# Kernel optimization log

Measured on AMD Instinct MI355X. Metric: run time of the kernel, lower is better.

The kernel has to match this reference:

```python
import jax, jax.numpy as jnp
import numpy as np

B, H, W, C = 16, 64, 64, 256
HEADS, WS, SHIFTS, QD = 8, 8, (0, 4), 512
N = WS * WS
HD = C // HEADS
MLP_H = 4 * C
DEPTH = 2
EPS = 1e-5


def _rel_pos_index():
    coords = np.stack(np.meshgrid(np.arange(WS), np.arange(WS), indexing='ij'))  # [2,ws,ws]
    flat = coords.reshape(2, -1)
    rel = (flat[:, :, None] - flat[:, None, :]).transpose(1, 2, 0)  # [N,N,2]
    rel[..., 0] += WS - 1
    rel[..., 1] += WS - 1
    rel[..., 0] *= 2 * WS - 1
    return jnp.asarray(rel.sum(-1))  # [N,N] int


def _shift_mask(shift):
    img = np.zeros((H, W))
    cnt = 0
    for hs in (slice(0, -WS), slice(-WS, -shift), slice(-shift, None)):
        for ws_ in (slice(0, -WS), slice(-WS, -shift), slice(-shift, None)):
            img[hs, ws_] = cnt
            cnt += 1
    mw = img.reshape(H // WS, WS, W // WS, WS).transpose(0, 2, 1, 3).reshape(-1, N)  # [nW,N]
    am = mw[:, None, :] - mw[:, :, None]
    return jnp.asarray(np.where(am != 0, -100.0, 0.0).astype(np.float32))  # [nW,N,N]


RPI = _rel_pos_index()


def layernorm(x, g, b):
    mu = x.mean(-1, keepdims=True)
    var = ((x - mu) ** 2).mean(-1, keepdims=True)
    return (x - mu) * jax.lax.rsqrt(var + EPS) * g + b


def window_partition(x):  # [B,H,W,C] -> [B*nW, N, C]
    x = x.reshape(B, H // WS, WS, W // WS, WS, C)
    return x.transpose(0, 1, 3, 2, 4, 5).reshape(-1, N, C)


def window_reverse(w):  # [B*nW, N, C] -> [B,H,W,C]
    x = w.reshape(B, H // WS, W // WS, WS, WS, C)
    return x.transpose(0, 1, 3, 2, 4, 5).reshape(B, H, W, C)


def swin_block(x, shift, n1g, n1b, qkvw, qkvb, rpb, pw, pb, n2g, n2b, f1w, f1b, f2w, f2b):
    shortcut = x
    y = layernorm(x, n1g, n1b).reshape(B, H, W, C)
    if shift > 0:
        y = jnp.roll(y, (-shift, -shift), axis=(1, 2))
    xw = window_partition(y)                                      # [B_, N, C]
    qkv = (xw @ qkvw + qkvb).reshape(-1, N, 3, HEADS, HD)
    q, k, v = (qkv[:, :, i].transpose(0, 2, 1, 3) for i in range(3))  # [B_,h,N,hd]
    scores = jnp.einsum('bhnd,bhmd->bhnm', q * (HD ** -0.5), k)
    bias = rpb[RPI].transpose(2, 0, 1)                            # [h,N,N]
    scores = scores + bias[None]
    if shift > 0:
        mask = _shift_mask(shift)                                 # [nW,N,N]
        nW = mask.shape[0]
        scores = scores.reshape(B, nW, HEADS, N, N) + mask[None, :, None]
        scores = scores.reshape(-1, HEADS, N, N)
    attn = jax.nn.softmax(scores, axis=-1)
    out = jnp.einsum('bhnm,bhmd->bhnd', attn, v).transpose(0, 2, 1, 3).reshape(-1, N, C)
    out = out @ pw + pb
    y = window_reverse(out)
    if shift > 0:
        y = jnp.roll(y, (shift, shift), axis=(1, 2))
    x = shortcut + y.reshape(B, H * W, C)
    h = layernorm(x, n2g, n2b)
    h = jax.nn.gelu(h @ f1w + f1b, approximate=False) @ f2w + f2b
    return x + h


def cross_attn(x, cond, cng, cnb, inw, inb, outw, outb):
    xn = layernorm(x, cng, cnb)
    q = xn @ inw[:C].T + inb[:C]
    k = cond @ inw[C:2 * C].T + inb[C:2 * C]
    v = cond @ inw[2 * C:].T + inb[2 * C:]
    Tq, Tk = q.shape[1], k.shape[1]
    q = q.reshape(B, Tq, HEADS, HD).transpose(0, 2, 1, 3) * (HD ** -0.5)
    k = k.reshape(B, Tk, HEADS, HD).transpose(0, 2, 1, 3)
    v = v.reshape(B, Tk, HEADS, HD).transpose(0, 2, 1, 3)
    a = jax.nn.softmax(jnp.einsum('bhqd,bhkd->bhqk', q, k), axis=-1)
    o = jnp.einsum('bhqk,bhkd->bhqd', a, v).transpose(0, 2, 1, 3).reshape(B, Tq, C)
    return x + o @ outw.T + outb


def setup_inputs() -> dict:
    key = jax.random.key(0)
    ks = iter(jax.random.split(key, 40))
    s = 0.02
    d = {
        'x': jax.random.normal(next(ks), (B, H * W, C), jnp.float32),
        'emb': jax.random.normal(next(ks), (B, 1, QD), jnp.float32),
        'qenc_w': jax.random.normal(next(ks), (QD, C)) * s,
        'qenc_b': jnp.zeros((C,)),
        'n1_g': jnp.ones((DEPTH, C)), 'n1_b': jnp.zeros((DEPTH, C)),
        'qkv_w': jax.random.normal(next(ks), (DEPTH, C, 3 * C)) * s,
        'qkv_b': jnp.zeros((DEPTH, 3 * C)),
        'rpb': jax.random.normal(next(ks), (DEPTH, (2 * WS - 1) ** 2, HEADS)) * s,
        'proj_w': jax.random.normal(next(ks), (DEPTH, C, C)) * s,
        'proj_b': jnp.zeros((DEPTH, C)),
        'n2_g': jnp.ones((DEPTH, C)), 'n2_b': jnp.zeros((DEPTH, C)),
        'fc1_w': jax.random.normal(next(ks), (DEPTH, C, MLP_H)) * s,
        'fc1_b': jnp.zeros((DEPTH, MLP_H)),
        'fc2_w': jax.random.normal(next(ks), (DEPTH, MLP_H, C)) * s,
        'fc2_b': jnp.zeros((DEPTH, C)),
        'cn_g': jnp.ones((DEPTH, C)), 'cn_b': jnp.zeros((DEPTH, C)),
        'ca_in_w': jax.random.normal(next(ks), (DEPTH, 3 * C, C)) * s,
        'ca_in_b': jnp.zeros((DEPTH, 3 * C)),
        'ca_out_w': jax.random.normal(next(ks), (DEPTH, C, C)) * s,
        'ca_out_b': jnp.zeros((DEPTH, C)),
    }
    return d


def reference(x, emb, qenc_w, qenc_b, n1_g, n1_b, qkv_w, qkv_b, rpb, proj_w, proj_b,
              n2_g, n2_b, fc1_w, fc1_b, fc2_w, fc2_b, cn_g, cn_b,
              ca_in_w, ca_in_b, ca_out_w, ca_out_b):
    for d in range(DEPTH):
        x = swin_block(x, SHIFTS[d], n1_g[d], n1_b[d], qkv_w[d], qkv_b[d], rpb[d],
                       proj_w[d], proj_b[d], n2_g[d], n2_b[d],
                       fc1_w[d], fc1_b[d], fc2_w[d], fc2_b[d])
        cond = emb @ qenc_w + qenc_b  # recomputed per block as in original
        x = cross_attn(x, cond, cn_g[d], cn_b[d], ca_in_w[d], ca_in_b[d],
                       ca_out_w[d], ca_out_b[d])
    return x
```

## Files before the change

### kernel.cpp

```cpp
#include <hip/hip_runtime.h>


typedef unsigned short bfraw;
typedef short s16x8 __attribute__((ext_vector_type(8)));
typedef short s16x4 __attribute__((ext_vector_type(4)));
typedef float f32x4 __attribute__((ext_vector_type(4)));

#define DEV static __device__ __forceinline__

DEV float b2f(int u){
  union { unsigned int i; float f; } x;
  x.i = ((unsigned int)u & 0xffffu) << 16;
  return x.f;
}
DEV unsigned short f2bbits(float f){
  union { float f; unsigned int i; } x; x.f = f;
  unsigned int i = x.i;
  unsigned int lsb = (i >> 16) & 1u;
  i += 0x7fffu + lsb;
  return (unsigned short)(i >> 16);
}
DEV unsigned int pkbf(float lo, float hi){
  unsigned int r;
  asm("v_cvt_pk_bf16_f32 %0, %1, %2" : "=v"(r) : "v"(lo), "v"(hi));
  return r;
}
DEV float gelu_tanh(float x){
  float t2 = 1.5957691216057308f * fmaf(0.044715f * x * x, x, x);
  float e = __expf(-t2);
  return x * __builtin_amdgcn_rcpf(1.f + e);
}

#define GLOAD_LDS16(g, l) __builtin_amdgcn_global_load_lds(                      \
    (const __attribute__((address_space(1))) void*)(g),                          \
    (__attribute__((address_space(3))) void*)(l), 16, 0, 0)

__global__ void k_tr(const float* __restrict__ in, bfraw* __restrict__ out, int K, int N){
  int idx = blockIdx.x * 256 + threadIdx.x;
  if (idx >= K * N) return;
  int n = idx / K, k = idx - n * K;
  out[idx] = f2bbits(in[(size_t)k * N + n]);
}

__global__ __launch_bounds__(256) void k_ln(
    const float* __restrict__ x, const float* __restrict__ g,
    const float* __restrict__ b, bfraw* __restrict__ y)
{
  const int lane = threadIdx.x & 63, wv = threadIdx.x >> 6;
  const size_t row = (size_t)blockIdx.x * 4 + wv;
  const float4 v = *(const float4*)(x + row * 256 + lane * 4);
  float s  = v.x + v.y + v.z + v.w;
  float s2 = v.x*v.x + v.y*v.y + v.z*v.z + v.w*v.w;
#pragma unroll
  for (int off = 32; off; off >>= 1){
    s  += __shfl_xor(s,  off);
    s2 += __shfl_xor(s2, off);
  }
  float mu  = s * (1.f/256.f);
  float var = s2 * (1.f/256.f) - mu * mu;
  float rs  = rsqrtf(var + 1e-5f);
  const float4 gv = *(const float4*)(g + lane * 4);
  const float4 bv = *(const float4*)(b + lane * 4);
  uint2 o;
  o.x = pkbf((v.x - mu) * rs * gv.x + bv.x, (v.y - mu) * rs * gv.y + bv.y);
  o.y = pkbf((v.z - mu) * rs * gv.z + bv.z, (v.w - mu) * rs * gv.w + bv.w);
  *(uint2*)(y + row * 256 + lane * 4) = o;
}

template<int EPI>
__global__ __launch_bounds__(256, 2) void k_gemm(
    const bfraw* __restrict__ A, const bfraw* __restrict__ Bt,
    const float* __restrict__ bias,
    bfraw* __restrict__ Cout, int ldc,
    float* __restrict__ xfp, const float* __restrict__ xin,
    const float* __restrict__ addv,
    int M, int N, int K, int shift)
{
  constexpr int BK = 64;
  __shared__ __align__(16) bfraw sA[128 * BK];
  __shared__ __align__(16) bfraw sB[128 * BK];
  const int tid = threadIdx.x, lane = tid & 63, w = tid >> 6;
  const int lo16 = lane & 15, hg = lane >> 4;
  const int nbm = M >> 7, nbn = N >> 7;
  const int nwg = nbm * nbn;
  const int bid = blockIdx.x;
  const int wgid = (bid & 7) * (nwg >> 3) + (bid >> 3);
  const int tn = wgid % nbn, tm = wgid / nbn;
  const int m0 = tm << 7, n0 = tn << 7;
  const int wm = w & 1, wn = w >> 1;
  f32x4 acc[4][4] = {};

  const int srow = (w << 5) + (lane >> 3);
  const int scol = (((lane & 7) ^ (lane >> 3)) << 3);
  const int ksw  = (lane & 7) << 3;
  const bfraw* gA = A  + (size_t)(m0 + srow) * K + scol;
  const bfraw* gB = Bt + (size_t)(n0 + srow) * K + scol;

  const int cb = n0 + (wn << 6) + 4 * hg;

  f32x4 bv4[4];
#pragma unroll
  for (int ni = 0; ni < 4; ++ni) bv4[ni] = *(const f32x4*)(bias + cb + ni * 16);
  size_t rowoff_[4];
  f32x4 pre[16], pav[4];
  if constexpr (EPI == 2 || EPI == 3){
#pragma unroll
    for (int mi = 0; mi < 4; ++mi){
      const int r = m0 + (wm << 6) + (mi << 4) + lo16;
      if constexpr (EPI == 2){
        int b_ = r >> 12, rem = r & 4095;
        int wi = rem >> 6, n_ = rem & 63;
        int gi = ((wi >> 3) * 8 + (n_ >> 3) + shift) & 63;
        int gj = ((wi & 7) * 8 + (n_ & 7) + shift) & 63;
        rowoff_[mi] = ((size_t)b_ << 12) + gi * 64 + gj;
      } else {
        rowoff_[mi] = (size_t)r;
      }
      const float* src = (EPI == 2 ? xin : (const float*)xfp) + rowoff_[mi] * 256 + cb;
#pragma unroll
      for (int ni = 0; ni < 4; ++ni)
        pre[mi * 4 + ni] = *(const f32x4*)(src + ni * 16);
    }
    if constexpr (EPI == 3){
      const float* av = addv + (size_t)(m0 >> 12) * 256 + cb;
#pragma unroll
      for (int ni = 0; ni < 4; ++ni) pav[ni] = *(const f32x4*)(av + ni * 16);
    }
  }

  for (int kt = 0; kt < K; kt += BK){
    __syncthreads();
#pragma unroll
    for (int i = 0; i < 4; ++i){
      GLOAD_LDS16(gA + (size_t)(i * 8) * K + kt, &sA[(w * 4 + i) * 512]);
      GLOAD_LDS16(gB + (size_t)(i * 8) * K + kt, &sB[(w * 4 + i) * 512]);
    }
    __syncthreads();
#pragma unroll
    for (int ks = 0; ks < 2; ++ks){
      const int ko = (ks * 32 + (hg << 3)) ^ ksw;
      s16x8 af[4], bfr[4];
#pragma unroll
      for (int i = 0; i < 4; ++i){
        af[i]  = *(const s16x8*)&sA[((wm << 6) + (i << 4) + lo16) * BK + ko];
        bfr[i] = *(const s16x8*)&sB[((wn << 6) + (i << 4) + lo16) * BK + ko];
      }
#pragma unroll
      for (int ni = 0; ni < 4; ++ni)
#pragma unroll
        for (int mi = 0; mi < 4; ++mi)
          acc[ni][mi] = __builtin_amdgcn_mfma_f32_16x16x32_bf16(
              bfr[ni], af[mi], acc[ni][mi], 0, 0, 0);
    }
  }

#pragma unroll
  for (int mi = 0; mi < 4; ++mi){
    if constexpr (EPI == 0 || EPI == 1){
      const int r = m0 + (wm << 6) + (mi << 4) + lo16;
      bfraw* crow = Cout + (size_t)r * ldc + cb;
#pragma unroll
      for (int ni = 0; ni < 4; ++ni){
        f32x4 v = acc[ni][mi] + bv4[ni];
        if constexpr (EPI == 1){
          v[0] = gelu_tanh(v[0]); v[1] = gelu_tanh(v[1]);
          v[2] = gelu_tanh(v[2]); v[3] = gelu_tanh(v[3]);
        }
        uint2 o = make_uint2(pkbf(v[0], v[1]), pkbf(v[2], v[3]));
        *(uint2*)(crow + ni * 16) = o;
      }
    } else if constexpr (EPI == 2){
      float* xo = xfp + rowoff_[mi] * 256 + cb;
#pragma unroll
      for (int ni = 0; ni < 4; ++ni)
        *(f32x4*)(xo + ni * 16) = acc[ni][mi] + bv4[ni] + pre[mi * 4 + ni];
    } else {
      float* xo = xfp + rowoff_[mi] * 256 + cb;
#pragma unroll
      for (int ni = 0; ni < 4; ++ni)
        *(f32x4*)(xo + ni * 16) = acc[ni][mi] + bv4[ni] + pre[mi * 4 + ni] + pav[ni];
    }
  }
}

__global__ __launch_bounds__(64) void k_bias(const float* __restrict__ rpb,
                                             float* __restrict__ biasPk)
{
  const int blk = blockIdx.x;
  const int d = blk >> 5, cls = (blk >> 3) & 3, h = blk & 7;
  const int l = threadIdx.x, lo16 = l & 15, hg = l >> 4;
  const float* rp = rpb + (size_t)d * 225 * 8;
  float* ob = biasPk + (((size_t)d * 4 + cls) * 8 + h) * 4096;
#pragma unroll
  for (int mi = 0; mi < 4; ++mi)
#pragma unroll
    for (int ni = 0; ni < 4; ++ni)
#pragma unroll
      for (int j = 0; j < 4; ++j){
        int k = 16 * mi + 4 * hg + j, q = 16 * ni + lo16;
        int qr = q >> 3, qc = q & 7, kr = k >> 3, kc = k & 7;
        float v = rp[((qr - kr + 7) * 15 + (qc - kc + 7)) * 8 + h];
        if (d == 1){
          int lq = ((cls >> 1) ? (qr < 4 ? 1 : 2) : 0) * 3 + ((cls & 1) ? (qc < 4 ? 1 : 2) : 0);
          int lk = ((cls >> 1) ? (kr < 4 ? 1 : 2) : 0) * 3 + ((cls & 1) ? (kc < 4 ? 1 : 2) : 0);
          if (lq != lk) v -= 100.f;
        }
        ob[(mi * 4 + ni) * 256 + l * 4 + j] = v;
      }
}

__global__ __launch_bounds__(64) void k_attn(
    const bfraw* __restrict__ qkv, const float* __restrict__ biasPk,
    bfraw* __restrict__ aout, int shift)
{
  __shared__ __align__(16) bfraw sV[64 * 32];
  __shared__ __align__(16) bfraw sP[64 * 64];
  const int win = blockIdx.x >> 3, h = blockIdx.x & 7;
  const int b = win >> 6, wr = (win >> 3) & 7, wc = win & 7;
  const int l = threadIdx.x, lo16 = l & 15, hg = l >> 4;

  auto grow_of = [&](int n) -> size_t {
    int gi = (wr * 8 + (n >> 3) + shift) & 63;
    int gj = (wc * 8 + (n & 7) + shift) & 63;
    return ((size_t)b << 12) + gi * 64 + gj;
  };

  s16x8 vreg[4];
#pragma unroll
  for (int i = 0; i < 4; ++i){
    int row = i * 16 + (l >> 2);
    vreg[i] = *(const s16x8*)(qkv + grow_of(row) * 768 + 512 + h * 32 + (l & 3) * 8);
  }
#pragma unroll
  for (int i = 0; i < 4; ++i)
    *(s16x8*)&sV[i * 512 + l * 8] = vreg[i];

  s16x8 aK[4], bQ[4];
#pragma unroll
  for (int t = 0; t < 4; ++t){
    const bfraw* base = qkv + grow_of(16 * t + lo16) * 768 + h * 32 + hg * 8;
    bQ[t] = *(const s16x8*)base;
    aK[t] = *(const s16x8*)(base + 256);
  }

  f32x4 acc[4][4] = {};
#pragma unroll
  for (int mi = 0; mi < 4; ++mi)
#pragma unroll
    for (int ni = 0; ni < 4; ++ni)
      acc[mi][ni] = __builtin_amdgcn_mfma_f32_16x16x32_bf16(aK[mi], bQ[ni], acc[mi][ni], 0, 0, 0);

  const int cls = ((wr == 7) ? 2 : 0) | ((wc == 7) ? 1 : 0);
  const float* bb = biasPk + ((size_t)(cls * 8 + h)) * 4096;
#pragma unroll
  for (int mi = 0; mi < 4; ++mi)
#pragma unroll
    for (int ni = 0; ni < 4; ++ni){
      f32x4 bv4 = *(const f32x4*)(bb + (mi * 4 + ni) * 256 + l * 4);
      acc[mi][ni] = acc[mi][ni] * 0.17677669529663689f + bv4;
    }

#pragma unroll
  for (int ni = 0; ni < 4; ++ni){
    float m = acc[0][ni][0];
#pragma unroll
    for (int mi = 0; mi < 4; ++mi)
#pragma unroll
      for (int j = 0; j < 4; ++j) m = fmaxf(m, acc[mi][ni][j]);
    m = fmaxf(m, __shfl_xor(m, 16));
    m = fmaxf(m, __shfl_xor(m, 32));
    float s = 0.f;
#pragma unroll
    for (int mi = 0; mi < 4; ++mi)
#pragma unroll
      for (int j = 0; j < 4; ++j){
        float e = __expf(acc[mi][ni][j] - m);
        acc[mi][ni][j] = e; s += e;
      }
    s += __shfl_xor(s, 16);
    s += __shfl_xor(s, 32);
    float inv = 1.f / s;
#pragma unroll
    for (int mi = 0; mi < 4; ++mi)
#pragma unroll
      for (int j = 0; j < 4; ++j) acc[mi][ni][j] *= inv;
  }

#pragma unroll
  for (int mi = 0; mi < 4; ++mi)
#pragma unroll
    for (int ni = 0; ni < 4; ++ni){
      unsigned int w0 = pkbf(acc[mi][ni][0], acc[mi][ni][1]);
      unsigned int w1 = pkbf(acc[mi][ni][2], acc[mi][ni][3]);
      int q = 16 * ni + lo16;
      int ad = (q * 128 + (16 * mi + 4 * hg) * 2) ^ ((q & 7) << 4);
      *(uint2*)((char*)sP + ad) = make_uint2(w0, w1);
    }

  asm volatile("s_waitcnt lgkmcnt(0)" ::: "memory");
  __builtin_amdgcn_sched_barrier(0);

  f32x4 opv[4][2] = {};
#pragma unroll
  for (int kt = 0; kt < 2; ++kt){
    s16x8 ap[4];
#pragma unroll
    for (int qi = 0; qi < 4; ++qi){
      int q = 16 * qi + lo16;
      int ad = (q * 128 + (kt * 32 + hg * 8) * 2) ^ ((q & 7) << 4);
      ap[qi] = *(const s16x8*)((const char*)sP + ad);
    }
    s16x8 vb[2];
#pragma unroll
    for (int nt = 0; nt < 2; ++nt)
#pragma unroll
      for (int e = 0; e < 8; ++e)
        vb[nt][e] = (short)sV[(kt * 32 + hg * 8 + e) * 32 + nt * 16 + lo16];
#pragma unroll
    for (int qi = 0; qi < 4; ++qi)
#pragma unroll
      for (int nt = 0; nt < 2; ++nt)
        opv[qi][nt] = __builtin_amdgcn_mfma_f32_16x16x32_bf16(ap[qi], vb[nt], opv[qi][nt], 0, 0, 0);
  }

  bfraw* ob = aout + ((size_t)win * 64) * 256 + h * 32 + lo16;
#pragma unroll
  for (int qi = 0; qi < 4; ++qi)
#pragma unroll
    for (int nt = 0; nt < 2; ++nt)
#pragma unroll
      for (int j = 0; j < 4; ++j)
        ob[(size_t)(16 * qi + 4 * hg + j) * 256 + nt * 16] = f2bbits(opv[qi][nt][j]);
}

__global__ __launch_bounds__(256) void k_addvec(
    const float* __restrict__ emb, const float* __restrict__ qw, const float* __restrict__ qb,
    const float* __restrict__ inw, const float* __restrict__ inb,
    const float* __restrict__ outw, const float* __restrict__ outb,
    float* __restrict__ addv)
{
  const int d = blockIdx.x >> 4, b = blockIdx.x & 15;
  const int j = threadIdx.x;
  __shared__ float sc[256], sv[256];
  float a = qb[j];
  for (int k = 0; k < 512; ++k) a = fmaf(emb[b * 512 + k], qw[k * 256 + j], a);
  sc[j] = a; __syncthreads();
  float v = inb[d * 768 + 512 + j];
  const float* wrp = inw + (size_t)d * 768 * 256 + (size_t)(512 + j) * 256;
  for (int k = 0; k < 256; ++k) v = fmaf(sc[k], wrp[k], v);
  sv[j] = v; __syncthreads();
  float o = outb[d * 256 + j];
  const float* wop = outw + (size_t)d * 65536 + (size_t)j * 256;
  for (int k = 0; k < 256; ++k) o = fmaf(sv[k], wop[k], o);
  addv[(size_t)(d * 16 + b) * 256 + j] = o;
}

extern "C" void kernel_launch(void* const* d_in, const int* in_sizes, int n_in,
                              void* d_out, int out_size, void* d_ws, size_t ws_size,
                              hipStream_t stream)
{
  (void)in_sizes; (void)n_in; (void)out_size; (void)ws_size;
  const float* x_in     = (const float*)d_in[0];
  const float* emb      = (const float*)d_in[1];
  const float* qenc_w   = (const float*)d_in[2];
  const float* qenc_b   = (const float*)d_in[3];
  const float* n1_g     = (const float*)d_in[4];
  const float* n1_b     = (const float*)d_in[5];
  const float* qkv_w    = (const float*)d_in[6];
  const float* qkv_b    = (const float*)d_in[7];
  const float* rpb      = (const float*)d_in[8];
  const float* proj_w   = (const float*)d_in[9];
  const float* proj_b   = (const float*)d_in[10];
  const float* n2_g     = (const float*)d_in[11];
  const float* n2_b     = (const float*)d_in[12];
  const float* fc1_w    = (const float*)d_in[13];
  const float* fc1_b    = (const float*)d_in[14];
  const float* fc2_w    = (const float*)d_in[15];
  const float* fc2_b    = (const float*)d_in[16];
  const float* ca_in_w  = (const float*)d_in[19];
  const float* ca_in_b  = (const float*)d_in[20];
  const float* ca_out_w = (const float*)d_in[21];
  const float* ca_out_b = (const float*)d_in[22];

  float* xfp  = (float*)d_out;
  char* ws = (char*)d_ws;
  bfraw* ybuf = (bfraw*)ws;
  bfraw* qkvb = (bfraw*)(ws + ((size_t)32 << 20));
  bfraw* wT   = (bfraw*)(ws + ((size_t)160 << 20));
  float* biasPk = (float*)(ws + ((size_t)166 << 20));

  bfraw *qkvT[2], *projT[2], *fc1T[2], *fc2T[2];
  size_t off = 0;
  for (int d = 0; d < 2; ++d){ qkvT[d] = wT + off; off += 768 * 256; }
  for (int d = 0; d < 2; ++d){ projT[d] = wT + off; off += 256 * 256; }
  for (int d = 0; d < 2; ++d){ fc1T[d] = wT + off; off += 1024 * 256; }
  for (int d = 0; d < 2; ++d){ fc2T[d] = wT + off; off += 256 * 1024; }
  float* addv = (float*)(wT + ((off + 1) & ~(size_t)1));

  for (int d = 0; d < 2; ++d){
    k_tr<<<(256 * 768  + 255) / 256, 256, 0, stream>>>(qkv_w  + (size_t)d * 256 * 768,  qkvT[d], 256, 768);
    k_tr<<<(256 * 256  + 255) / 256, 256, 0, stream>>>(proj_w + (size_t)d * 256 * 256,  projT[d], 256, 256);
    k_tr<<<(256 * 1024 + 255) / 256, 256, 0, stream>>>(fc1_w  + (size_t)d * 256 * 1024, fc1T[d], 256, 1024);
    k_tr<<<(1024 * 256 + 255) / 256, 256, 0, stream>>>(fc2_w  + (size_t)d * 1024 * 256, fc2T[d], 1024, 256);
  }
  k_bias<<<64, 64, 0, stream>>>(rpb, biasPk);
  k_addvec<<<32, 256, 0, stream>>>(emb, qenc_w, qenc_b, ca_in_w, ca_in_b, ca_out_w, ca_out_b, addv);

  for (int d = 0; d < 2; ++d){
    const int shift = d ? 4 : 0;
    const float* resid_in = d ? (const float*)xfp : x_in;
    k_ln<<<16384, 256, 0, stream>>>(resid_in, n1_g + d * 256, n1_b + d * 256, ybuf);
    k_gemm<0><<<512 * 6, 256, 0, stream>>>(ybuf, qkvT[d], qkv_b + d * 768, qkvb, 768,
                                           nullptr, nullptr, nullptr, 65536, 768, 256, 0);
    k_attn<<<8192, 64, 0, stream>>>(qkvb, biasPk + (size_t)d * 4 * 8 * 4096, ybuf, shift);
    k_gemm<2><<<512 * 2, 256, 0, stream>>>(ybuf, projT[d], proj_b + d * 256, nullptr, 0,
                                           xfp, resid_in, nullptr, 65536, 256, 256, shift);
    k_ln<<<16384, 256, 0, stream>>>(xfp, n2_g + d * 256, n2_b + d * 256, ybuf);
    k_gemm<1><<<512 * 8, 256, 0, stream>>>(ybuf, fc1T[d], fc1_b + d * 1024, qkvb, 1024,
                                           nullptr, nullptr, nullptr, 65536, 1024, 256, 0);
    k_gemm<3><<<512 * 2, 256, 0, stream>>>(qkvb, fc2T[d], fc2_b + d * 256, nullptr, 0,
                                           xfp, nullptr, addv + (size_t)d * 16 * 256,
                                           65536, 256, 1024, 0);
  }
}
```

Measured before the change: 687.9 us.

## Fuse MLP fc1+GELU+fc2 into one kernel keeping hidden activations in LDS

Replaces the two MLP GEMM launches with a single k_mlp kernel. Each block processes 64 rows, computes the fc1 hidden chunk with GELU into LDS, and accumulates fc2 directly, then adds bias, the cross-attention vector and the residual. This removes the global write and read of the large 4C hidden tensor. In exchange, weights are loaded from global memory per warp without LDS staging, and there are fewer, larger blocks.

```diff
diff --git a/kernel.cpp b/kernel.cpp
--- a/kernel.cpp
+++ b/kernel.cpp
@@ -73,7 +73,6 @@
     const float* __restrict__ bias,
     bfraw* __restrict__ Cout, int ldc,
     float* __restrict__ xfp, const float* __restrict__ xin,
-    const float* __restrict__ addv,
     int M, int N, int K, int shift)
 {
   constexpr int BK = 64;
@@ -102,29 +101,20 @@
 #pragma unroll
   for (int ni = 0; ni < 4; ++ni) bv4[ni] = *(const f32x4*)(bias + cb + ni * 16);
   size_t rowoff_[4];
-  f32x4 pre[16], pav[4];
-  if constexpr (EPI == 2 || EPI == 3){
+  f32x4 pre[16];
+  if constexpr (EPI == 2){
 #pragma unroll
     for (int mi = 0; mi < 4; ++mi){
       const int r = m0 + (wm << 6) + (mi << 4) + lo16;
-      if constexpr (EPI == 2){
-        int b_ = r >> 12, rem = r & 4095;
-        int wi = rem >> 6, n_ = rem & 63;
-        int gi = ((wi >> 3) * 8 + (n_ >> 3) + shift) & 63;
-        int gj = ((wi & 7) * 8 + (n_ & 7) + shift) & 63;
-        rowoff_[mi] = ((size_t)b_ << 12) + gi * 64 + gj;
-      } else {
-        rowoff_[mi] = (size_t)r;
-      }
-      const float* src = (EPI == 2 ? xin : (const float*)xfp) + rowoff_[mi] * 256 + cb;
+      int b_ = r >> 12, rem = r & 4095;
+      int wi = rem >> 6, n_ = rem & 63;
+      int gi = ((wi >> 3) * 8 + (n_ >> 3) + shift) & 63;
+      int gj = ((wi & 7) * 8 + (n_ & 7) + shift) & 63;
+      rowoff_[mi] = ((size_t)b_ << 12) + gi * 64 + gj;
+      const float* src = xin + rowoff_[mi] * 256 + cb;
 #pragma unroll
       for (int ni = 0; ni < 4; ++ni)
         pre[mi * 4 + ni] = *(const f32x4*)(src + ni * 16);
-    }
-    if constexpr (EPI == 3){
-      const float* av = addv + (size_t)(m0 >> 12) * 256 + cb;
-#pragma unroll
-      for (int ni = 0; ni < 4; ++ni) pav[ni] = *(const f32x4*)(av + ni * 16);
     }
   }
 
@@ -156,30 +146,126 @@
 
 #pragma unroll
   for (int mi = 0; mi < 4; ++mi){
-    if constexpr (EPI == 0 || EPI == 1){
+    if constexpr (EPI == 0){
       const int r = m0 + (wm << 6) + (mi << 4) + lo16;
       bfraw* crow = Cout + (size_t)r * ldc + cb;
 #pragma unroll
       for (int ni = 0; ni < 4; ++ni){
         f32x4 v = acc[ni][mi] + bv4[ni];
-        if constexpr (EPI == 1){
-          v[0] = gelu_tanh(v[0]); v[1] = gelu_tanh(v[1]);
-          v[2] = gelu_tanh(v[2]); v[3] = gelu_tanh(v[3]);
-        }
         uint2 o = make_uint2(pkbf(v[0], v[1]), pkbf(v[2], v[3]));
         *(uint2*)(crow + ni * 16) = o;
       }
-    } else if constexpr (EPI == 2){
+    } else {
       float* xo = xfp + rowoff_[mi] * 256 + cb;
 #pragma unroll
       for (int ni = 0; ni < 4; ++ni)
         *(f32x4*)(xo + ni * 16) = acc[ni][mi] + bv4[ni] + pre[mi * 4 + ni];
-    } else {
-      float* xo = xfp + rowoff_[mi] * 256 + cb;
+    }
+  }
+}
+
+__global__ __launch_bounds__(256, 2) void k_mlp(
+    const bfraw* __restrict__ y,
+    const bfraw* __restrict__ w1t,
+    const float* __restrict__ b1,
+    const bfraw* __restrict__ w2t,
+    const float* __restrict__ b2,
+    float* __restrict__ xfp,
+    const float* __restrict__ addv)
+{
+  __shared__ __align__(16) bfraw yl[64 * 256];
+  __shared__ __align__(16) bfraw hl[64 * 128];
+  const int tid = threadIdx.x, lane = tid & 63, w = tid >> 6;
+  const int lo16 = lane & 15, hg = lane >> 4;
+  const int rb = blockIdx.x << 6;
+
+  {
+    const int l5 = lane >> 5, c8 = lane & 31;
+#pragma unroll
+    for (int i = 0; i < 8; ++i){
+      int r0 = i * 8 + w * 2;
+      int row = r0 + l5;
+      int col = (c8 * 8) ^ ((row & 7) << 3);
+      GLOAD_LDS16(y + (size_t)(rb + row) * 256 + col, &yl[r0 * 256]);
+    }
+  }
+
+  f32x4 acc2[4][4] = {};
+  __syncthreads();
+
+  for (int c = 0; c < 8; ++c){
+    f32x4 acc1[2][4] = {};
+#pragma unroll
+    for (int kk = 0; kk < 8; ++kk){
+      s16x8 bf1[2], af[4];
+#pragma unroll
+      for (int t = 0; t < 2; ++t)
+        bf1[t] = *(const s16x8*)(w1t + (size_t)(c * 128 + w * 32 + t * 16 + lo16) * 256
+                                 + kk * 32 + hg * 8);
+#pragma unroll
+      for (int mi = 0; mi < 4; ++mi){
+        int row = mi * 16 + lo16;
+        af[mi] = *(const s16x8*)&yl[row * 256 + ((kk * 32 + hg * 8) ^ ((row & 7) << 3))];
+      }
+#pragma unroll
+      for (int t = 0; t < 2; ++t)
+#pragma unroll
+        for (int mi = 0; mi < 4; ++mi)
+          acc1[t][mi] = __builtin_amdgcn_mfma_f32_16x16x32_bf16(
+              bf1[t], af[mi], acc1[t][mi], 0, 0, 0);
+    }
+#pragma unroll
+    for (int t = 0; t < 2; ++t){
+      const f32x4 b1v = *(const f32x4*)(b1 + c * 128 + w * 32 + t * 16 + 4 * hg);
+#pragma unroll
+      for (int mi = 0; mi < 4; ++mi){
+        int row = mi * 16 + lo16;
+        float v0 = gelu_tanh(acc1[t][mi][0] + b1v[0]);
+        float v1 = gelu_tanh(acc1[t][mi][1] + b1v[1]);
+        float v2 = gelu_tanh(acc1[t][mi][2] + b1v[2]);
+        float v3 = gelu_tanh(acc1[t][mi][3] + b1v[3]);
+        int col = (w * 32 + t * 16 + 4 * hg) ^ ((row & 7) << 3);
+        *(uint2*)&hl[row * 128 + col] = make_uint2(pkbf(v0, v1), pkbf(v2, v3));
+      }
+    }
+    __syncthreads();
+#pragma unroll
+    for (int kk = 0; kk < 4; ++kk){
+      s16x8 bf2[4], af2[4];
 #pragma unroll
       for (int ni = 0; ni < 4; ++ni)
-        *(f32x4*)(xo + ni * 16) = acc[ni][mi] + bv4[ni] + pre[mi * 4 + ni] + pav[ni];
-    }
+        bf2[ni] = *(const s16x8*)(w2t + (size_t)(w * 64 + ni * 16 + lo16) * 1024
+                                  + c * 128 + kk * 32 + hg * 8);
+#pragma unroll
+      for (int mi = 0; mi < 4; ++mi){
+        int row = mi * 16 + lo16;
+        af2[mi] = *(const s16x8*)&hl[row * 128 + ((kk * 32 + hg * 8) ^ ((row & 7) << 3))];
+      }
+#pragma unroll
+      for (int ni = 0; ni < 4; ++ni)
+#pragma unroll
+        for (int mi = 0; mi < 4; ++mi)
+          acc2[ni][mi] = __builtin_amdgcn_mfma_f32_16x16x32_bf16(
+              bf2[ni], af2[mi], acc2[ni][mi], 0, 0, 0);
+    }
+    __syncthreads();
+  }
+
+  const int cb = w * 64 + 4 * hg;
+  const int bidx = rb >> 12;
+  f32x4 b2v[4], av[4];
+#pragma unroll
+  for (int ni = 0; ni < 4; ++ni){
+    b2v[ni] = *(const f32x4*)(b2 + cb + ni * 16);
+    av[ni]  = *(const f32x4*)(addv + bidx * 256 + cb + ni * 16);
+  }
+#pragma unroll
+  for (int mi = 0; mi < 4; ++mi){
+    const size_t r = (size_t)rb + mi * 16 + lo16;
+    float* xo = xfp + r * 256 + cb;
+#pragma unroll
+    for (int ni = 0; ni < 4; ++ni)
+      *(f32x4*)(xo + ni * 16) = acc2[ni][mi] + b2v[ni] + av[ni] + *(const f32x4*)(xo + ni * 16);
   }
 }
 
@@ -411,15 +497,13 @@
     const float* resid_in = d ? (const float*)xfp : x_in;
     k_ln<<<16384, 256, 0, stream>>>(resid_in, n1_g + d * 256, n1_b + d * 256, ybuf);
     k_gemm<0><<<512 * 6, 256, 0, stream>>>(ybuf, qkvT[d], qkv_b + d * 768, qkvb, 768,
-                                           nullptr, nullptr, nullptr, 65536, 768, 256, 0);
+                                           nullptr, nullptr, 65536, 768, 256, 0);
     k_attn<<<8192, 64, 0, stream>>>(qkvb, biasPk + (size_t)d * 4 * 8 * 4096, ybuf, shift);
     k_gemm<2><<<512 * 2, 256, 0, stream>>>(ybuf, projT[d], proj_b + d * 256, nullptr, 0,
-                                           xfp, resid_in, nullptr, 65536, 256, 256, shift);
+                                           xfp, resid_in, 65536, 256, 256, shift);
     k_ln<<<16384, 256, 0, stream>>>(xfp, n2_g + d * 256, n2_b + d * 256, ybuf);
-    k_gemm<1><<<512 * 8, 256, 0, stream>>>(ybuf, fc1T[d], fc1_b + d * 1024, qkvb, 1024,
-                                           nullptr, nullptr, nullptr, 65536, 1024, 256, 0);
-    k_gemm<3><<<512 * 2, 256, 0, stream>>>(qkvb, fc2T[d], fc2_b + d * 256, nullptr, 0,
-                                           xfp, nullptr, addv + (size_t)d * 16 * 256,
-                                           65536, 256, 1024, 0);
-  }
-}
+    k_mlp<<<1024, 256, 0, stream>>>(ybuf, fc1T[d], fc1_b + d * 1024,
+                                    fc2T[d], fc2_b + d * 256,
+                                    xfp, addv + (size_t)d * 16 * 256);
+  }
+}
```

Measured after the change: 752.4 us. +9.4%, slower.

## Fuse LayerNorm into qkv and fc1 GEMM prologues

Applied to the files above, without the earlier changes.

Replaces the standalone LayerNorm kernels with a GEMM variant that loads the fp32 activation rows, normalizes them in registers and writes a full 128x256 bf16 A tile into swizzled LDS before the K loop. This removes two kernel launches per block and the bf16 intermediate round trip through global memory. In exchange, each output-column tile recomputes LayerNorm and re-reads the fp32 rows, and the larger LDS footprint can reduce occupancy. The generic GEMM drops its bf16-output epilogues.

```diff
diff --git a/kernel.cpp b/kernel.cpp
--- a/kernel.cpp
+++ b/kernel.cpp
@@ -3,7 +3,6 @@
 
 typedef unsigned short bfraw;
 typedef short s16x8 __attribute__((ext_vector_type(8)));
-typedef short s16x4 __attribute__((ext_vector_type(4)));
 typedef float f32x4 __attribute__((ext_vector_type(4)));
 
 #define DEV static __device__ __forceinline__
@@ -42,36 +41,124 @@
   out[idx] = f2bbits(in[(size_t)k * N + n]);
 }
 
-__global__ __launch_bounds__(256) void k_ln(
-    const float* __restrict__ x, const float* __restrict__ g,
-    const float* __restrict__ b, bfraw* __restrict__ y)
-{
-  const int lane = threadIdx.x & 63, wv = threadIdx.x >> 6;
-  const size_t row = (size_t)blockIdx.x * 4 + wv;
-  const float4 v = *(const float4*)(x + row * 256 + lane * 4);
-  float s  = v.x + v.y + v.z + v.w;
-  float s2 = v.x*v.x + v.y*v.y + v.z*v.z + v.w*v.w;
-#pragma unroll
-  for (int off = 32; off; off >>= 1){
-    s  += __shfl_xor(s,  off);
-    s2 += __shfl_xor(s2, off);
-  }
-  float mu  = s * (1.f/256.f);
-  float var = s2 * (1.f/256.f) - mu * mu;
-  float rs  = rsqrtf(var + 1e-5f);
-  const float4 gv = *(const float4*)(g + lane * 4);
-  const float4 bv = *(const float4*)(b + lane * 4);
-  uint2 o;
-  o.x = pkbf((v.x - mu) * rs * gv.x + bv.x, (v.y - mu) * rs * gv.y + bv.y);
-  o.y = pkbf((v.z - mu) * rs * gv.z + bv.z, (v.w - mu) * rs * gv.w + bv.w);
-  *(uint2*)(y + row * 256 + lane * 4) = o;
+template<int EPI>
+__global__ __launch_bounds__(256, 2) void k_gemm_ln(
+    const float* __restrict__ Afp, const float* __restrict__ lng,
+    const float* __restrict__ lnb,
+    const bfraw* __restrict__ Bt, const float* __restrict__ bias,
+    bfraw* __restrict__ Cout, int ldc, int M, int N)
+{
+  constexpr int K = 256, BK = 64;
+  __shared__ __align__(16) bfraw sA[128 * 256];
+  __shared__ __align__(16) bfraw sB[128 * BK];
+  const int tid = threadIdx.x, lane = tid & 63, w = tid >> 6;
+  const int lo16 = lane & 15, hg = lane >> 4;
+  const int nbm = M >> 7, nbn = N >> 7;
+  const int nwg = nbm * nbn;
+  const int bid = blockIdx.x;
+  const int wgid = (bid & 7) * (nwg >> 3) + (bid >> 3);
+  const int tn = wgid % nbn, tm = wgid / nbn;
+  const int m0 = tm << 7, n0 = tn << 7;
+  const int wm = w & 1, wn = w >> 1;
+
+  {
+    const int rg = lane >> 3;
+    const int c0 = (lane & 7) * 32;
+    f32x4 gv[8], ev[8];
+#pragma unroll
+    for (int t = 0; t < 8; ++t){
+      gv[t] = *(const f32x4*)(lng + c0 + t * 4);
+      ev[t] = *(const f32x4*)(lnb + c0 + t * 4);
+    }
+#pragma unroll
+    for (int i = 0; i < 4; ++i){
+      const int row = (w << 5) + rg + (i << 3);
+      const float* src = Afp + (size_t)(m0 + row) * 256 + c0;
+      f32x4 a[8];
+      float s = 0.f, s2 = 0.f;
+#pragma unroll
+      for (int t = 0; t < 8; ++t){
+        a[t] = *(const f32x4*)(src + t * 4);
+#pragma unroll
+        for (int e = 0; e < 4; ++e){ s += a[t][e]; s2 += a[t][e] * a[t][e]; }
+      }
+      s += __shfl_xor(s, 1); s2 += __shfl_xor(s2, 1);
+      s += __shfl_xor(s, 2); s2 += __shfl_xor(s2, 2);
+      s += __shfl_xor(s, 4); s2 += __shfl_xor(s2, 4);
+      float mu = s * (1.f / 256.f);
+      float rs = rsqrtf(s2 * (1.f / 256.f) - mu * mu + 1e-5f);
+      const int sw = (row & 7) << 3;
+#pragma unroll
+      for (int u = 0; u < 4; ++u){
+        uint4 o;
+        o.x = pkbf((a[2*u][0] - mu) * rs * gv[2*u][0] + ev[2*u][0],
+                   (a[2*u][1] - mu) * rs * gv[2*u][1] + ev[2*u][1]);
+        o.y = pkbf((a[2*u][2] - mu) * rs * gv[2*u][2] + ev[2*u][2],
+                   (a[2*u][3] - mu) * rs * gv[2*u][3] + ev[2*u][3]);
+        o.z = pkbf((a[2*u+1][0] - mu) * rs * gv[2*u+1][0] + ev[2*u+1][0],
+                   (a[2*u+1][1] - mu) * rs * gv[2*u+1][1] + ev[2*u+1][1]);
+        o.w = pkbf((a[2*u+1][2] - mu) * rs * gv[2*u+1][2] + ev[2*u+1][2],
+                   (a[2*u+1][3] - mu) * rs * gv[2*u+1][3] + ev[2*u+1][3]);
+        *(uint4*)&sA[row * 256 + ((c0 + u * 8) ^ sw)] = o;
+      }
+    }
+  }
+
+  f32x4 acc[4][4] = {};
+  const int srow = (w << 5) + (lane >> 3);
+  const int scol = (((lane & 7) ^ (lane >> 3)) << 3);
+  const bfraw* gB = Bt + (size_t)(n0 + srow) * K + scol;
+  const int cb = n0 + (wn << 6) + 4 * hg;
+  f32x4 bv4[4];
+#pragma unroll
+  for (int ni = 0; ni < 4; ++ni) bv4[ni] = *(const f32x4*)(bias + cb + ni * 16);
+
+  for (int kt = 0; kt < K; kt += BK){
+    __syncthreads();
+#pragma unroll
+    for (int i = 0; i < 4; ++i)
+      GLOAD_LDS16(gB + (size_t)(i * 8) * K + kt, &sB[(w * 4 + i) * 512]);
+    __syncthreads();
+#pragma unroll
+    for (int ks = 0; ks < 2; ++ks){
+      const int ko2 = ks * 32 + (hg << 3);
+      const int ko  = ko2 ^ ((lane & 7) << 3);
+      s16x8 af[4], bfr[4];
+#pragma unroll
+      for (int i = 0; i < 4; ++i){
+        const int rowA = (wm << 6) + (i << 4) + lo16;
+        af[i]  = *(const s16x8*)&sA[rowA * 256 + ((kt + ko2) ^ ((rowA & 7) << 3))];
+        bfr[i] = *(const s16x8*)&sB[(((wn << 6) + (i << 4) + lo16)) * BK + ko];
+      }
+#pragma unroll
+      for (int ni = 0; ni < 4; ++ni)
+#pragma unroll
+        for (int mi = 0; mi < 4; ++mi)
+          acc[ni][mi] = __builtin_amdgcn_mfma_f32_16x16x32_bf16(
+              bfr[ni], af[mi], acc[ni][mi], 0, 0, 0);
+    }
+  }
+
+#pragma unroll
+  for (int mi = 0; mi < 4; ++mi){
+    const int r = m0 + (wm << 6) + (mi << 4) + lo16;
+    bfraw* crow = Cout + (size_t)r * ldc + cb;
+#pragma unroll
+    for (int ni = 0; ni < 4; ++ni){
+      f32x4 v = acc[ni][mi] + bv4[ni];
+      if constexpr (EPI == 1){
+        v[0] = gelu_tanh(v[0]); v[1] = gelu_tanh(v[1]);
+        v[2] = gelu_tanh(v[2]); v[3] = gelu_tanh(v[3]);
+      }
+      *(uint2*)(crow + ni * 16) = make_uint2(pkbf(v[0], v[1]), pkbf(v[2], v[3]));
+    }
+  }
 }
 
 template<int EPI>
 __global__ __launch_bounds__(256, 2) void k_gemm(
     const bfraw* __restrict__ A, const bfraw* __restrict__ Bt,
     const float* __restrict__ bias,
-    bfraw* __restrict__ Cout, int ldc,
     float* __restrict__ xfp, const float* __restrict__ xin,
     const float* __restrict__ addv,
     int M, int N, int K, int shift)
@@ -103,29 +190,27 @@
   for (int ni = 0; ni < 4; ++ni) bv4[ni] = *(const f32x4*)(bias + cb + ni * 16);
   size_t rowoff_[4];
   f32x4 pre[16], pav[4];
-  if constexpr (EPI == 2 || EPI == 3){
-#pragma unroll
-    for (int mi = 0; mi < 4; ++mi){
-      const int r = m0 + (wm << 6) + (mi << 4) + lo16;
-      if constexpr (EPI == 2){
-        int b_ = r >> 12, rem = r & 4095;
-        int wi = rem >> 6, n_ = rem & 63;
-        int gi = ((wi >> 3) * 8 + (n_ >> 3) + shift) & 63;
-        int gj = ((wi & 7) * 8 + (n_ & 7) + shift) & 63;
-        rowoff_[mi] = ((size_t)b_ << 12) + gi * 64 + gj;
-      } else {
-        rowoff_[mi] = (size_t)r;
-      }
-      const float* src = (EPI == 2 ? xin : (const float*)xfp) + rowoff_[mi] * 256 + cb;
-#pragma unroll
-      for (int ni = 0; ni < 4; ++ni)
-        pre[mi * 4 + ni] = *(const f32x4*)(src + ni * 16);
-    }
-    if constexpr (EPI == 3){
-      const float* av = addv + (size_t)(m0 >> 12) * 256 + cb;
-#pragma unroll
-      for (int ni = 0; ni < 4; ++ni) pav[ni] = *(const f32x4*)(av + ni * 16);
-    }
+#pragma unroll
+  for (int mi = 0; mi < 4; ++mi){
+    const int r = m0 + (wm << 6) + (mi << 4) + lo16;
+    if constexpr (EPI == 2){
+      int b_ = r >> 12, rem = r & 4095;
+      int wi = rem >> 6, n_ = rem & 63;
+      int gi = ((wi >> 3) * 8 + (n_ >> 3) + shift) & 63;
+      int gj = ((wi & 7) * 8 + (n_ & 7) + shift) & 63;
+      rowoff_[mi] = ((size_t)b_ << 12) + gi * 64 + gj;
+    } else {
+      rowoff_[mi] = (size_t)r;
+    }
+    const float* src = (EPI == 2 ? xin : (const float*)xfp) + rowoff_[mi] * 256 + cb;
+#pragma unroll
+    for (int ni = 0; ni < 4; ++ni)
+      pre[mi * 4 + ni] = *(const f32x4*)(src + ni * 16);
+  }
+  if constexpr (EPI == 3){
+    const float* av = addv + (size_t)(m0 >> 12) * 256 + cb;
+#pragma unroll
+    for (int ni = 0; ni < 4; ++ni) pav[ni] = *(const f32x4*)(av + ni * 16);
   }
 
   for (int kt = 0; kt < K; kt += BK){
@@ -156,26 +241,12 @@
 
 #pragma unroll
   for (int mi = 0; mi < 4; ++mi){
-    if constexpr (EPI == 0 || EPI == 1){
-      const int r = m0 + (wm << 6) + (mi << 4) + lo16;
-      bfraw* crow = Cout + (size_t)r * ldc + cb;
-#pragma unroll
-      for (int ni = 0; ni < 4; ++ni){
-        f32x4 v = acc[ni][mi] + bv4[ni];
-        if constexpr (EPI == 1){
-          v[0] = gelu_tanh(v[0]); v[1] = gelu_tanh(v[1]);
-          v[2] = gelu_tanh(v[2]); v[3] = gelu_tanh(v[3]);
-        }
-        uint2 o = make_uint2(pkbf(v[0], v[1]), pkbf(v[2], v[3]));
-        *(uint2*)(crow + ni * 16) = o;
-      }
-    } else if constexpr (EPI == 2){
-      float* xo = xfp + rowoff_[mi] * 256 + cb;
+    float* xo = xfp + rowoff_[mi] * 256 + cb;
+    if constexpr (EPI == 2){
 #pragma unroll
       for (int ni = 0; ni < 4; ++ni)
         *(f32x4*)(xo + ni * 16) = acc[ni][mi] + bv4[ni] + pre[mi * 4 + ni];
     } else {
-      float* xo = xfp + rowoff_[mi] * 256 + cb;
 #pragma unroll
       for (int ni = 0; ni < 4; ++ni)
         *(f32x4*)(xo + ni * 16) = acc[ni][mi] + bv4[ni] + pre[mi * 4 + ni] + pav[ni];
@@ -409,16 +480,14 @@
   for (int d = 0; d < 2; ++d){
     const int shift = d ? 4 : 0;
     const float* resid_in = d ? (const float*)xfp : x_in;
-    k_ln<<<16384, 256, 0, stream>>>(resid_in, n1_g + d * 256, n1_b + d * 256, ybuf);
-    k_gemm<0><<<512 * 6, 256, 0, stream>>>(ybuf, qkvT[d], qkv_b + d * 768, qkvb, 768,
-                                           nullptr, nullptr, nullptr, 65536, 768, 256, 0);
+    k_gemm_ln<0><<<512 * 6, 256, 0, stream>>>(resid_in, n1_g + d * 256, n1_b + d * 256,
+                                              qkvT[d], qkv_b + d * 768, qkvb, 768, 65536, 768);
     k_attn<<<8192, 64, 0, stream>>>(qkvb, biasPk + (size_t)d * 4 * 8 * 4096, ybuf, shift);
-    k_gemm<2><<<512 * 2, 256, 0, stream>>>(ybuf, projT[d], proj_b + d * 256, nullptr, 0,
+    k_gemm<2><<<512 * 2, 256, 0, stream>>>(ybuf, projT[d], proj_b + d * 256,
                                            xfp, resid_in, nullptr, 65536, 256, 256, shift);
-    k_ln<<<16384, 256, 0, stream>>>(xfp, n2_g + d * 256, n2_b + d * 256, ybuf);
-    k_gemm<1><<<512 * 8, 256, 0, stream>>>(ybuf, fc1T[d], fc1_b + d * 1024, qkvb, 1024,
-                                           nullptr, nullptr, nullptr, 65536, 1024, 256, 0);
-    k_gemm<3><<<512 * 2, 256, 0, stream>>>(qkvb, fc2T[d], fc2_b + d * 256, nullptr, 0,
+    k_gemm_ln<1><<<512 * 8, 256, 0, stream>>>(xfp, n2_g + d * 256, n2_b + d * 256,
+                                              fc1T[d], fc1_b + d * 1024, qkvb, 1024, 65536, 1024);
+    k_gemm<3><<<512 * 2, 256, 0, stream>>>(qkvb, fc2T[d], fc2_b + d * 256,
                                            xfp, nullptr, addv + (size_t)d * 16 * 256,
                                            65536, 256, 1024, 0);
   }
```

Result: slower. 878.0 us (+27.6%).

## Double-buffer GEMM shared-memory tiles to overlap global loads with MFMA

Applied to the files above, without the earlier changes.

The GEMM main loop now uses two LDS buffers per operand and issues the global-to-LDS loads for tile t+1 before computing tile t. A partial vmcnt wait plus an s_barrier replaces the two __syncthreads per iteration. The aim is to hide global memory latency behind the MFMA work. In exchange LDS use doubles to 64KB per block, which may reduce occupancy at launch_bounds(256,2), and correctness depends on the hand-set vmcnt count matching the number of outstanding loads.

```diff
diff --git a/kernel.cpp b/kernel.cpp
--- a/kernel.cpp
+++ b/kernel.cpp
@@ -3,7 +3,6 @@
 
 typedef unsigned short bfraw;
 typedef short s16x8 __attribute__((ext_vector_type(8)));
-typedef short s16x4 __attribute__((ext_vector_type(4)));
 typedef float f32x4 __attribute__((ext_vector_type(4)));
 
 #define DEV static __device__ __forceinline__
@@ -77,8 +76,8 @@
     int M, int N, int K, int shift)
 {
   constexpr int BK = 64;
-  __shared__ __align__(16) bfraw sA[128 * BK];
-  __shared__ __align__(16) bfraw sB[128 * BK];
+  __shared__ __align__(16) bfraw sA[2][128 * BK];
+  __shared__ __align__(16) bfraw sB[2][128 * BK];
   const int tid = threadIdx.x, lane = tid & 63, w = tid >> 6;
   const int lo16 = lane & 15, hg = lane >> 4;
   const int nbm = M >> 7, nbn = N >> 7;
@@ -128,22 +127,35 @@
     }
   }
 
-  for (int kt = 0; kt < K; kt += BK){
-    __syncthreads();
-#pragma unroll
-    for (int i = 0; i < 4; ++i){
-      GLOAD_LDS16(gA + (size_t)(i * 8) * K + kt, &sA[(w * 4 + i) * 512]);
-      GLOAD_LDS16(gB + (size_t)(i * 8) * K + kt, &sB[(w * 4 + i) * 512]);
-    }
-    __syncthreads();
+  const int nt = K >> 6;
+#pragma unroll
+  for (int i = 0; i < 4; ++i){
+    GLOAD_LDS16(gA + (size_t)(i * 8) * K, &sA[0][(w * 4 + i) * 512]);
+    GLOAD_LDS16(gB + (size_t)(i * 8) * K, &sB[0][(w * 4 + i) * 512]);
+  }
+  for (int t = 0; t < nt; ++t){
+    const int cur = t & 1;
+    if (t + 1 < nt){
+      const int nxt = cur ^ 1, kt = (t + 1) << 6;
+#pragma unroll
+      for (int i = 0; i < 4; ++i){
+        GLOAD_LDS16(gA + (size_t)(i * 8) * K + kt, &sA[nxt][(w * 4 + i) * 512]);
+        GLOAD_LDS16(gB + (size_t)(i * 8) * K + kt, &sB[nxt][(w * 4 + i) * 512]);
+      }
+      asm volatile("s_waitcnt vmcnt(8)" ::: "memory");
+    } else {
+      asm volatile("s_waitcnt vmcnt(0)" ::: "memory");
+    }
+    __builtin_amdgcn_s_barrier();
+    __builtin_amdgcn_sched_barrier(0);
 #pragma unroll
     for (int ks = 0; ks < 2; ++ks){
       const int ko = (ks * 32 + (hg << 3)) ^ ksw;
       s16x8 af[4], bfr[4];
 #pragma unroll
       for (int i = 0; i < 4; ++i){
-        af[i]  = *(const s16x8*)&sA[((wm << 6) + (i << 4) + lo16) * BK + ko];
-        bfr[i] = *(const s16x8*)&sB[((wn << 6) + (i << 4) + lo16) * BK + ko];
+        af[i]  = *(const s16x8*)&sA[cur][((wm << 6) + (i << 4) + lo16) * BK + ko];
+        bfr[i] = *(const s16x8*)&sB[cur][((wn << 6) + (i << 4) + lo16) * BK + ko];
       }
 #pragma unroll
       for (int ni = 0; ni < 4; ++ni)
@@ -152,6 +164,9 @@
           acc[ni][mi] = __builtin_amdgcn_mfma_f32_16x16x32_bf16(
               bfr[ni], af[mi], acc[ni][mi], 0, 0, 0);
     }
+    asm volatile("s_waitcnt lgkmcnt(0)" ::: "memory");
+    __builtin_amdgcn_s_barrier();
+    __builtin_amdgcn_sched_barrier(0);
   }
 
 #pragma unroll
@@ -166,8 +181,7 @@
           v[0] = gelu_tanh(v[0]); v[1] = gelu_tanh(v[1]);
           v[2] = gelu_tanh(v[2]); v[3] = gelu_tanh(v[3]);
         }
-        uint2 o = make_uint2(pkbf(v[0], v[1]), pkbf(v[2], v[3]));
-        *(uint2*)(crow + ni * 16) = o;
+        *(uint2*)(crow + ni * 16) = make_uint2(pkbf(v[0], v[1]), pkbf(v[2], v[3]));
       }
     } else if constexpr (EPI == 2){
       float* xo = xfp + rowoff_[mi] * 256 + cb;
```

New measurement: 699.1 us. No clear change (+1.6%).
